# Optimization experiments

Hardware: AMD Instinct MI355X
Metric: run time of the kernel (lower is better)

The kernel has to match this reference:

```python
import jax, jax.numpy as jnp
import numpy as np

N, IN_DIM, H1, NHEAD = 8192, 768, 128, 2
H1T = NHEAD * H1          # 256: each AttentionLayer output dim
H2, H3, OUT = 128, 128, 64
K = H1T + 1 - H2          # 129: conv kernel width
E_PAIRS = 100000
ALPHA = 0.2
NEG = -9e15


def _l2norm(x):
    # F.normalize(p=2, dim=1)
    return x / jnp.maximum(jnp.linalg.norm(x, axis=1, keepdims=True), 1e-12)


def _gat_block(h, adj_mask, a, act):
    # h: [N, D]; a: [2D, 1]; dense NxN GAT attention, masked softmax, aggregate
    D = h.shape[1]
    wh1 = h @ a[:D]            # [N,1]
    wh2 = h @ a[D:]            # [N,1]
    e = act(wh1 + wh2.T)       # [N,N]
    att = jnp.where(adj_mask, e, NEG)
    att = jax.nn.softmax(att, axis=1)   # dropout omitted (eval/deterministic)
    return att @ h             # [N,D]


def _attention_layer(x, adj_mask, W, a, b):
    h = x @ W                  # [N, H1T]
    hp = _gat_block(h, adj_mask, a, lambda z: jax.nn.leaky_relu(z, negative_slope=ALPHA))
    return _l2norm(jax.nn.elu(hp)) + b


def setup_inputs() -> dict:
    key = jax.random.key(0)
    ks = jax.random.split(key, 16)
    g = 1.414

    def xavier(k, shape):
        fan_in, fan_out = shape[-2], shape[-1]
        bound = g * np.sqrt(6.0 / (fan_in + fan_out))
        return jax.random.uniform(k, shape, jnp.float32, -bound, bound)

    x = jax.random.normal(ks[0], (N, IN_DIM), jnp.float32)
    adj = jax.random.randint(ks[1], (N, N), 0, 2, jnp.int32)
    train_sample = jax.random.randint(ks[2], (E_PAIRS, 2), 0, N, jnp.int32)

    return {
        "x": x, "adj": adj, "train_sample": train_sample,
        # per-head GAT params (stacked over heads)
        "head_W": xavier(ks[3], (NHEAD, IN_DIM, H1T)),
        "head_a": xavier(ks[4], (NHEAD, 2 * H1T, 1)),
        "head_b": jnp.zeros((NHEAD, H1T), jnp.float32),
        # Conv attention layer
        "conv_w": jax.random.normal(ks[5], (1, 1, 1, K), jnp.float32) * (1.0 / np.sqrt(K)),
        "conv_cb": jnp.zeros((1,), jnp.float32),
        "conv_a": xavier(ks[6], (2 * H2, 1)),
        "conv_b": jnp.zeros((H2,), jnp.float32),
        # decoder MLPs (stored as [in, out])
        "tf_w1": xavier(ks[7], (H2, H3)), "tf_b1": jnp.zeros((H3,), jnp.float32),
        "tf_w2": xavier(ks[8], (H3, OUT)), "tf_b2": jnp.zeros((OUT,), jnp.float32),
        "tg_w1": xavier(ks[9], (H2, H3)), "tg_b1": jnp.zeros((H3,), jnp.float32),
        "tg_w2": xavier(ks[10], (H3, OUT)), "tg_b2": jnp.zeros((OUT,), jnp.float32),
    }


def reference(x, adj, train_sample, head_W, head_a, head_b,
              conv_w, conv_cb, conv_a, conv_b,
              tf_w1, tf_b1, tf_w2, tf_b2, tg_w1, tg_b1, tg_w2, tg_b2):
    adj_mask = adj > 0

    # Layer 1: mean over attention heads, then elu
    heads = jax.vmap(_attention_layer, in_axes=(None, None, 0, 0, 0))(
        x, adj_mask, head_W, head_a, head_b)           # [NHEAD, N, H1T]
    z = jax.nn.elu(jnp.mean(heads, axis=0))            # [N, H1T]

    # Conv layer: 1x129 conv sliding over feature axis -> [N, H2]
    zi = z[None, None, :, :]                           # [1,1,N,H1T]
    hc = jax.lax.conv_general_dilated(
        zi, conv_w, window_strides=(1, 1), padding="VALID",
        dimension_numbers=("NCHW", "OIHW", "NCHW"))
    h = hc[0, 0] + conv_cb[0]                          # [N, H2]

    hp = _gat_block(h, adj_mask, conv_a, jax.nn.elu)
    embed = _l2norm(jax.nn.elu(hp)) + conv_b           # [N, H2]

    # decoders (dropout p=0.01 omitted for deterministic reference)
    tf = jax.nn.elu(jax.nn.elu(embed @ tf_w1 + tf_b1) @ tf_w2 + tf_b2)
    tg = jax.nn.elu(jax.nn.elu(embed @ tg_w1 + tg_b1) @ tg_w2 + tg_b2)

    pred = jnp.sum(tf[train_sample[:, 0]] * tg[train_sample[:, 1]], axis=1, keepdims=True)
    return pred
```

## Files before the change

kernel.cpp:

```cpp
#include <hip/hip_runtime.h>


typedef _Float16 f16;
typedef _Float16 f16x8 __attribute__((ext_vector_type(8)));
typedef float f32x4 __attribute__((ext_vector_type(4)));

#define DEV __device__ __forceinline__
#define L2E 1.4426950408889634f
#define NN 8192
#define IND 768
#define D1 256
#define DT 512
#define D2 128
#define KC 129
#define EPAIRS 100000

#if __has_builtin(__builtin_amdgcn_exp2f)
#define EXP2(x) __builtin_amdgcn_exp2f(x)
#else
#define EXP2(x) exp2f(x)
#endif

DEV float eluf(float x){ return x > 0.f ? x : EXP2(x*L2E) - 1.f; }

__global__ __launch_bounds__(256) void k_pack(const int4* __restrict__ adj4, unsigned* __restrict__ maskw){
  int idx = blockIdx.x*256 + threadIdx.x;
  int4 v = adj4[idx];
  unsigned n = (unsigned)(v.x > 0) | ((unsigned)(v.y > 0) << 1)
             | ((unsigned)(v.z > 0) << 2) | ((unsigned)(v.w > 0) << 3);
  n |= __shfl_xor(n, 1) << 4;
  n |= __shfl_xor(n, 2) << 8;
  n |= __shfl_xor(n, 4) << 16;
  if ((threadIdx.x & 7) == 0) maskw[idx >> 3] = n;
}

__global__ __launch_bounds__(256) void k_cast_x(const float* __restrict__ x, f16* __restrict__ x16){
  int i = (blockIdx.x*256 + threadIdx.x)*4;
  float4 v = *(const float4*)(x + i);
  union { f16 h[4]; uint2 u; } p;
  p.h[0]=(f16)v.x; p.h[1]=(f16)v.y; p.h[2]=(f16)v.z; p.h[3]=(f16)v.w;
  *(uint2*)(x16 + i) = p.u;
}

__global__ __launch_bounds__(256) void k_wt(const float* __restrict__ W, f16* __restrict__ Wt){
  int np = blockIdx.x; int h = np >> 8, d = np & 255;
  for (int k = threadIdx.x; k < IND; k += 256)
    Wt[(size_t)np*IND + k] = (f16)W[((size_t)h*IND + k)*D1 + d];
}

__global__ __launch_bounds__(256) void k_gemm_h(
    const f16* __restrict__ x16, const f16* __restrict__ Wt,
    const float* __restrict__ head_a,
    f16* __restrict__ hT, float* __restrict__ wh1, float* __restrict__ wh2){
  __shared__ f16 As[64*72];
  __shared__ f16 Bs[128*72];
  int m0 = blockIdx.x*64, n0 = blockIdx.y*128;
  int t = threadIdx.x, lane = t & 63, w = t >> 6;
  int wi = w >> 1, wd = w & 1;
  int rm = lane & 15, qm = (lane >> 4)*8;
  f32x4 acc[2][4] = {};
  for (int k0 = 0; k0 < IND; k0 += 64){
#pragma unroll
    for (int p = 0; p < 2; p++){
      int idx = p*256 + t, r = idx >> 3, cc = (idx & 7)*8;
      *(uint4*)&As[r*72 + cc] = *(const uint4*)&x16[(size_t)(m0 + r)*IND + k0 + cc];
    }
#pragma unroll
    for (int p = 0; p < 4; p++){
      int idx = p*256 + t, r = idx >> 3, cc = (idx & 7)*8;
      *(uint4*)&Bs[r*72 + cc] = *(const uint4*)&Wt[(size_t)(n0 + r)*IND + k0 + cc];
    }
    __syncthreads();
#pragma unroll
    for (int ks = 0; ks < 2; ks++){
      f16x8 a0 = *(const f16x8*)&As[(wi*32 + rm)*72 + ks*32 + qm];
      f16x8 a1 = *(const f16x8*)&As[(wi*32 + 16 + rm)*72 + ks*32 + qm];
#pragma unroll
      for (int fn = 0; fn < 4; fn++){
        f16x8 b = *(const f16x8*)&Bs[(wd*64 + fn*16 + rm)*72 + ks*32 + qm];
        acc[0][fn] = __builtin_amdgcn_mfma_f32_16x16x32_f16(a0, b, acc[0][fn], 0, 0, 0);
        acc[1][fn] = __builtin_amdgcn_mfma_f32_16x16x32_f16(a1, b, acc[1][fn], 0, 0, 0);
      }
    }
    __syncthreads();
  }
  int quad = lane >> 4, cl = lane & 15;
  int head = n0 >> 8;
  float a1v[4], a2v[4];
#pragma unroll
  for (int fn = 0; fn < 4; fn++){
    int d = (n0 & 255) + wd*64 + fn*16 + cl;
    a1v[fn] = head_a[head*DT + d];
    a2v[fn] = head_a[head*DT + D1 + d];
  }
  float p1[2][4], p2[2][4];
#pragma unroll
  for (int fi = 0; fi < 2; fi++){
#pragma unroll
    for (int fn = 0; fn < 4; fn++){
      int npg = n0 + wd*64 + fn*16 + cl;
      int mg = m0 + wi*32 + fi*16 + quad*4;
      union { f16 h[4]; uint2 u; } pk;
#pragma unroll
      for (int reg = 0; reg < 4; reg++) pk.h[reg] = (f16)acc[fi][fn][reg];
      *(uint2*)&hT[(size_t)npg*NN + mg] = pk.u;
    }
#pragma unroll
    for (int reg = 0; reg < 4; reg++){
      float s1 = 0.f, s2 = 0.f;
#pragma unroll
      for (int fn = 0; fn < 4; fn++){ s1 += acc[fi][fn][reg]*a1v[fn]; s2 += acc[fi][fn][reg]*a2v[fn]; }
      p1[fi][reg] = s1; p2[fi][reg] = s2;
    }
  }
#pragma unroll
  for (int o = 1; o < 16; o <<= 1){
#pragma unroll
    for (int fi = 0; fi < 2; fi++)
#pragma unroll
      for (int reg = 0; reg < 4; reg++){
        p1[fi][reg] += __shfl_xor(p1[fi][reg], o);
        p2[fi][reg] += __shfl_xor(p2[fi][reg], o);
      }
  }
  if (cl == 0){
#pragma unroll
    for (int fi = 0; fi < 2; fi++)
#pragma unroll
      for (int reg = 0; reg < 4; reg++){
        int mg = m0 + wi*32 + fi*16 + quad*4 + reg;
        atomicAdd(&wh1[head*NN + mg], p1[fi][reg]);
        atomicAdd(&wh2[head*NN + mg], p2[fi][reg]);
      }
  }
}

__global__ __launch_bounds__(256) void k_gmax(const float* __restrict__ wh2, unsigned* __restrict__ gmax){
  int h = blockIdx.y;
  int i = blockIdx.x*256 + threadIdx.x;
  float v = wh2[h*NN + i];
#pragma unroll
  for (int o = 32; o > 0; o >>= 1) v = fmaxf(v, __shfl_xor(v, o));
  if ((threadIdx.x & 63) == 0){
    unsigned b = __float_as_uint(v);
    unsigned enc = (b & 0x80000000u) ? ~b : (b | 0x80000000u);
    atomicMax(gmax + h, enc);
  }
}

__global__ __launch_bounds__(256) void k_colterms(const float* __restrict__ wh2,
                                                  float* __restrict__ c1, float* __restrict__ c2){
  int i = blockIdx.x*256 + threadIdx.x;
  float v = wh2[i]*L2E;
  c1[i] = v; c2[i] = 0.2f*v;
}

__global__ __launch_bounds__(256) void k_agg_head(
    const f16* __restrict__ hT, const unsigned* __restrict__ maskw,
    const float* __restrict__ wh1, const float* __restrict__ c1,
    const float* __restrict__ c2, const unsigned* __restrict__ gmaxp,
    float* __restrict__ num, float* __restrict__ den){
  __shared__ f16 Hs[256*72];
  __shared__ f16 Ws[64*72];
  __shared__ float rowa[64], rowb[64];
  int head = blockIdx.z;
  int i0 = blockIdx.x*64;
  int jbase = blockIdx.y*4096;
  const f16* hTh = hT + (size_t)head*D1*NN;
  int t = threadIdx.x, lane = t & 63, w = t >> 6;
  int rm = lane & 15, qm = (lane >> 4)*8;
  if (t < 64){
    unsigned e = gmaxp[head];
    float gmax = __uint_as_float((e & 0x80000000u) ? (e ^ 0x80000000u) : ~e);
    float u = wh1[head*NN + i0 + t];
    float sm = u + gmax;
    float M = (sm > 0.f ? sm : 0.2f*sm)*L2E;
    rowa[t] = u*L2E - M;
    rowb[t] = 0.2f*u*L2E - M;
  }
  __syncthreads();
  int si = t >> 2, sjq = (t & 3)*16;
  float ra = rowa[si], rb = rowb[si];
  const float* c1h = c1 + head*NN;
  const float* c2h = c2 + head*NN;
  const unsigned* mrowp = maskw + (size_t)(i0 + si)*(NN/32);
  float rden = 0.f;
  f32x4 acc[4][4] = {};
  for (int j0 = 0; j0 < 4096; j0 += 64){
    int jg = jbase + j0;
#pragma unroll
    for (int p = 0; p < 8; p++){
      int idx = p*256 + t, dr = idx >> 3, cc = (idx & 7)*8;
      *(uint4*)&Hs[dr*72 + cc] = *(const uint4*)&hTh[(size_t)dr*NN + jg + cc];
    }
    unsigned mb = mrowp[(jg + sjq) >> 5] >> (sjq & 31);
    float ca[16], cb[16];
#pragma unroll
    for (int k = 0; k < 4; k++){
      float4 va = *(const float4*)&c1h[jg + sjq + 4*k];
      float4 vb = *(const float4*)&c2h[jg + sjq + 4*k];
      ca[4*k]=va.x; ca[4*k+1]=va.y; ca[4*k+2]=va.z; ca[4*k+3]=va.w;
      cb[4*k]=vb.x; cb[4*k+1]=vb.y; cb[4*k+2]=vb.z; cb[4*k+3]=vb.w;
    }
    f16x8 wlo, whi;
    float dsum = 0.f;
#pragma unroll
    for (int q = 0; q < 16; q++){
      float s1 = ra + ca[q], s2 = rb + cb[q];
      float wv = EXP2(fmaxf(s1, s2));
      wv = ((mb >> q) & 1u) ? wv : 0.f;
      dsum += wv;
      if (q < 8) wlo[q] = (f16)wv; else whi[q - 8] = (f16)wv;
    }
    *(f16x8*)&Ws[si*72 + sjq]     = wlo;
    *(f16x8*)&Ws[si*72 + sjq + 8] = whi;
    dsum += __shfl_xor(dsum, 1);
    dsum += __shfl_xor(dsum, 2);
    rden += dsum;
    __syncthreads();
#pragma unroll
    for (int ks = 0; ks < 2; ks++){
      f16x8 a[4], b[4];
#pragma unroll
      for (int mi = 0; mi < 4; mi++) a[mi] = *(const f16x8*)&Ws[(mi*16 + rm)*72 + ks*32 + qm];
#pragma unroll
      for (int fn = 0; fn < 4; fn++) b[fn] = *(const f16x8*)&Hs[(w*64 + fn*16 + rm)*72 + ks*32 + qm];
#pragma unroll
      for (int mi = 0; mi < 4; mi++)
#pragma unroll
        for (int fn = 0; fn < 4; fn++)
          acc[mi][fn] = __builtin_amdgcn_mfma_f32_16x16x32_f16(a[mi], b[fn], acc[mi][fn], 0, 0, 0);
    }
    __syncthreads();
  }
  if ((t & 3) == 0) atomicAdd(&den[head*NN + i0 + si], rden);
  int quad = lane >> 4, cl = lane & 15;
#pragma unroll
  for (int mi = 0; mi < 4; mi++)
#pragma unroll
    for (int fn = 0; fn < 4; fn++){
      int rr = i0 + mi*16 + quad*4;
      int dc = w*64 + fn*16 + cl;
#pragma unroll
      for (int reg = 0; reg < 4; reg++)
        atomicAdd(&num[((size_t)head*NN + rr + reg)*D1 + dc], acc[mi][fn][reg]);
    }
}

__global__ __launch_bounds__(256) void k_merge_conv(
    const float* __restrict__ num, const float* __restrict__ den,
    const float* __restrict__ head_b, const float* __restrict__ conv_w,
    const float* __restrict__ conv_cb, const float* __restrict__ conv_a,
    f16* __restrict__ gT, float* __restrict__ wc1L, float* __restrict__ wc2L){
  __shared__ float zrow[2][256];
  __shared__ float cw[KC];
  __shared__ float ca[256];
  __shared__ float red[2][2];
  __shared__ float red2[2][2][2];
  int t = threadIdx.x, g = t >> 7, c = t & 127;
  int r = blockIdx.x*2 + g;
  if (t < KC) cw[t] = conv_w[t];
  ca[t] = conv_a[t];
  float zv0 = 0.f, zv1 = 0.f;
#pragma unroll
  for (int h = 0; h < 2; h++){
    const float* nr = num + ((size_t)h*NN + r)*D1;
    float inv = 1.f / den[h*NN + r];
    float e0 = eluf(nr[c]*inv);
    float e1 = eluf(nr[c + 128]*inv);
    float ss = e0*e0 + e1*e1;
#pragma unroll
    for (int o = 32; o > 0; o >>= 1) ss += __shfl_xor(ss, o);
    if ((t & 63) == 0) red[g][(t >> 6) & 1] = ss;
    __syncthreads();
    float invn = 1.f / fmaxf(sqrtf(red[g][0] + red[g][1]), 1e-12f);
    zv0 += e0*invn + head_b[h*D1 + c];
    zv1 += e1*invn + head_b[h*D1 + 128 + c];
    __syncthreads();
  }
  zrow[g][c]       = eluf(0.5f*zv0);
  zrow[g][c + 128] = eluf(0.5f*zv1);
  __syncthreads();
  float s = conv_cb[0];
  for (int k = 0; k < KC; k++) s += zrow[g][c + k]*cw[k];
  gT[(size_t)c*NN + r] = (f16)s;
  float p1 = s*ca[c], p2 = s*ca[128 + c];
#pragma unroll
  for (int o = 32; o > 0; o >>= 1){ p1 += __shfl_xor(p1, o); p2 += __shfl_xor(p2, o); }
  if ((t & 63) == 0){ red2[g][(t >> 6) & 1][0] = p1; red2[g][(t >> 6) & 1][1] = p2; }
  __syncthreads();
  if ((t & 127) == 0){
    wc1L[r] = (red2[g][0][0] + red2[g][1][0])*L2E;
    wc2L[r] = (red2[g][0][1] + red2[g][1][1])*L2E;
  }
}

__global__ __launch_bounds__(256) void k_agg_conv(
    const f16* __restrict__ gT, const unsigned* __restrict__ maskw,
    const float* __restrict__ wc1L, const float* __restrict__ wc2L,
    float* __restrict__ num, float* __restrict__ den){
  __shared__ f16 Hs[128*72];
  __shared__ f16 Ws[64*72];
  __shared__ float rowc[64];
  int i0 = blockIdx.x*64;
  int jbase = blockIdx.y*1024;
  int t = threadIdx.x, lane = t & 63, w = t >> 6;
  int rm = lane & 15, qm = (lane >> 4)*8;
  if (t < 64) rowc[t] = wc1L[i0 + t];
  __syncthreads();
  int si = t >> 2, sjq = (t & 3)*16;
  float ra = rowc[si];
  const unsigned* mrowp = maskw + (size_t)(i0 + si)*(NN/32);
  float rden = 0.f;
  f32x4 acc[4][2] = {};
  for (int j0 = 0; j0 < 1024; j0 += 64){
    int jg = jbase + j0;
#pragma unroll
    for (int p = 0; p < 4; p++){
      int idx = p*256 + t, dr = idx >> 3, cc = (idx & 7)*8;
      *(uint4*)&Hs[dr*72 + cc] = *(const uint4*)&gT[(size_t)dr*NN + jg + cc];
    }
    unsigned mb = mrowp[(jg + sjq) >> 5] >> (sjq & 31);
    float ca[16];
#pragma unroll
    for (int k = 0; k < 4; k++){
      float4 va = *(const float4*)&wc2L[jg + sjq + 4*k];
      ca[4*k]=va.x; ca[4*k+1]=va.y; ca[4*k+2]=va.z; ca[4*k+3]=va.w;
    }
    f16x8 wlo, whi;
    float dsum = 0.f;
#pragma unroll
    for (int q = 0; q < 16; q++){
      float sL = ra + ca[q];
      float t2 = EXP2(sL);
      float wv = sL > 0.f ? t2 : EXP2((t2 - 1.f)*L2E);
      wv = ((mb >> q) & 1u) ? wv : 0.f;
      dsum += wv;
      if (q < 8) wlo[q] = (f16)wv; else whi[q - 8] = (f16)wv;
    }
    *(f16x8*)&Ws[si*72 + sjq]     = wlo;
    *(f16x8*)&Ws[si*72 + sjq + 8] = whi;
    dsum += __shfl_xor(dsum, 1);
    dsum += __shfl_xor(dsum, 2);
    rden += dsum;
    __syncthreads();
#pragma unroll
    for (int ks = 0; ks < 2; ks++){
      f16x8 a[4], b[2];
#pragma unroll
      for (int mi = 0; mi < 4; mi++) a[mi] = *(const f16x8*)&Ws[(mi*16 + rm)*72 + ks*32 + qm];
#pragma unroll
      for (int fn = 0; fn < 2; fn++) b[fn] = *(const f16x8*)&Hs[(w*32 + fn*16 + rm)*72 + ks*32 + qm];
#pragma unroll
      for (int mi = 0; mi < 4; mi++)
#pragma unroll
        for (int fn = 0; fn < 2; fn++)
          acc[mi][fn] = __builtin_amdgcn_mfma_f32_16x16x32_f16(a[mi], b[fn], acc[mi][fn], 0, 0, 0);
    }
    __syncthreads();
  }
  if ((t & 3) == 0) atomicAdd(&den[i0 + si], rden);
  int quad = lane >> 4, cl = lane & 15;
#pragma unroll
  for (int mi = 0; mi < 4; mi++)
#pragma unroll
    for (int fn = 0; fn < 2; fn++){
      int rr = i0 + mi*16 + quad*4;
      int dc = w*32 + fn*16 + cl;
#pragma unroll
      for (int reg = 0; reg < 4; reg++)
        atomicAdd(&num[(size_t)(rr + reg)*D2 + dc], acc[mi][fn][reg]);
    }
}

__global__ __launch_bounds__(256) void k_embed(
    const float* __restrict__ numc, const float* __restrict__ denc,
    const float* __restrict__ conv_b, float* __restrict__ embed){
  __shared__ float red[2][2];
  int t = threadIdx.x, g = t >> 7, c = t & 127;
  int r = blockIdx.x*2 + g;
  float e = eluf(numc[(size_t)r*D2 + c] / denc[r]);
  float ss = e*e;
#pragma unroll
  for (int o = 32; o > 0; o >>= 1) ss += __shfl_xor(ss, o);
  if ((t & 63) == 0) red[g][(t >> 6) & 1] = ss;
  __syncthreads();
  float invn = 1.f / fmaxf(sqrtf(red[g][0] + red[g][1]), 1e-12f);
  embed[(size_t)r*D2 + c] = e*invn + conv_b[c];
}

__global__ __launch_bounds__(256) void k_mlp(
    const float* __restrict__ embed,
    const float* __restrict__ fw1, const float* __restrict__ fb1,
    const float* __restrict__ fw2, const float* __restrict__ fb2,
    const float* __restrict__ gw1, const float* __restrict__ gb1,
    const float* __restrict__ gw2, const float* __restrict__ gb2,
    float* __restrict__ tf, float* __restrict__ tg){
  const float* w1 = blockIdx.y ? gw1 : fw1;
  const float* b1 = blockIdx.y ? gb1 : fb1;
  const float* w2 = blockIdx.y ? gw2 : fw2;
  const float* b2 = blockIdx.y ? gb2 : fb2;
  float* out = blockIdx.y ? tg : tf;
  int t = threadIdx.x;
  int c = t & 127, kh = t >> 7;
  int o = t & 63, kh2 = t >> 6;
  float rw1[64];
#pragma unroll
  for (int i = 0; i < 64; i++) rw1[i] = w1[(kh*64 + i)*128 + c];
  float rw2[32];
#pragma unroll
  for (int i = 0; i < 32; i++) rw2[i] = w2[(kh2*32 + i)*64 + o];
  float bb1 = b1[c], bb2 = b2[o];
  __shared__ float erow[4][128];
  __shared__ float hidp[2][4][128];
  __shared__ float hid[4][128];
  __shared__ float outp[4][4][64];
  int r0 = blockIdx.x*32;
  for (int it = 0; it < 8; it++){
    int rbase = r0 + it*4;
    ((float2*)erow)[t] = ((const float2*)(embed + (size_t)rbase*128))[t];
    __syncthreads();
#pragma unroll
    for (int g = 0; g < 4; g++){
      float s = 0.f;
#pragma unroll
      for (int i = 0; i < 64; i++) s += erow[g][kh*64 + i]*rw1[i];
      hidp[kh][g][c] = s;
    }
    __syncthreads();
#pragma unroll
    for (int gg = 0; gg < 2; gg++){
      int g = kh + 2*gg;
      hid[g][c] = eluf(bb1 + hidp[0][g][c] + hidp[1][g][c]);
    }
    __syncthreads();
#pragma unroll
    for (int g = 0; g < 4; g++){
      float s = 0.f;
#pragma unroll
      for (int i = 0; i < 32; i++) s += hid[g][kh2*32 + i]*rw2[i];
      outp[kh2][g][o] = s;
    }
    __syncthreads();
    { int g = t >> 6;
      out[(size_t)(rbase + g)*64 + o] =
        eluf(bb2 + outp[0][g][o] + outp[1][g][o] + outp[2][g][o] + outp[3][g][o]); }
    __syncthreads();
  }
}

__global__ __launch_bounds__(256) void k_pred(
    const int* __restrict__ ts, const float4* __restrict__ tf4,
    const float4* __restrict__ tg4, float* __restrict__ out){
  int p = blockIdx.x*16 + (threadIdx.x >> 4);
  int l = threadIdx.x & 15;
  int i = ts[2*p], j = ts[2*p + 1];
  float4 a = tf4[(size_t)i*16 + l], b = tg4[(size_t)j*16 + l];
  float v = a.x*b.x + a.y*b.y + a.z*b.z + a.w*b.w;
  v += __shfl_xor(v, 1); v += __shfl_xor(v, 2);
  v += __shfl_xor(v, 4); v += __shfl_xor(v, 8);
  if (l == 0) out[p] = v;
}

#define OFF_MASK  ((size_t)0)
#define OFF_X16   ((size_t)8388608)
#define OFF_WT16  ((size_t)20971520)
#define OFF_HT16  ((size_t)21757952)
#define OFF_WH1   ((size_t)30146560)
#define OFF_WH2   ((size_t)30212096)
#define OFF_C1    ((size_t)30277632)
#define OFF_C2    ((size_t)30343168)
#define OFF_GMAX  ((size_t)30408704)
#define OFF_NUM1  ((size_t)30408960)
#define OFF_DEN1  ((size_t)47186176)
#define OFF_GT16  ((size_t)47251712)
#define OFF_WC1L  ((size_t)49348864)
#define OFF_WC2L  ((size_t)49381632)
#define OFF_NUMC  ((size_t)49414400)
#define OFF_DENC  ((size_t)53608704)
#define OFF_EMB   ((size_t)53641472)
#define OFF_TF    ((size_t)57835776)
#define OFF_TG    ((size_t)59932928)

extern "C" void kernel_launch(void* const* d_in, const int* in_sizes, int n_in,
                              void* d_out, int out_size, void* d_ws, size_t ws_size,
                              hipStream_t stream){
  const float* x      = (const float*)d_in[0];
  const int*   adj    = (const int*)d_in[1];
  const int*   ts     = (const int*)d_in[2];
  const float* head_W = (const float*)d_in[3];
  const float* head_a = (const float*)d_in[4];
  const float* head_b = (const float*)d_in[5];
  const float* conv_w = (const float*)d_in[6];
  const float* conv_cb= (const float*)d_in[7];
  const float* conv_a = (const float*)d_in[8];
  const float* conv_b = (const float*)d_in[9];
  const float* tf_w1  = (const float*)d_in[10];
  const float* tf_b1  = (const float*)d_in[11];
  const float* tf_w2  = (const float*)d_in[12];
  const float* tf_b2  = (const float*)d_in[13];
  const float* tg_w1  = (const float*)d_in[14];
  const float* tg_b1  = (const float*)d_in[15];
  const float* tg_w2  = (const float*)d_in[16];
  const float* tg_b2  = (const float*)d_in[17];
  float* outp = (float*)d_out;
  char* ws = (char*)d_ws;

  unsigned* maskw = (unsigned*)(ws + OFF_MASK);
  f16*   x16   = (f16*)(ws + OFF_X16);
  f16*   Wt16  = (f16*)(ws + OFF_WT16);
  f16*   hT16  = (f16*)(ws + OFF_HT16);
  float* wh1   = (float*)(ws + OFF_WH1);
  float* wh2   = (float*)(ws + OFF_WH2);
  float* c1    = (float*)(ws + OFF_C1);
  float* c2    = (float*)(ws + OFF_C2);
  unsigned* gmax = (unsigned*)(ws + OFF_GMAX);
  float* num1  = (float*)(ws + OFF_NUM1);
  float* den1  = (float*)(ws + OFF_DEN1);
  f16*   gT16  = (f16*)(ws + OFF_GT16);
  float* wc1L  = (float*)(ws + OFF_WC1L);
  float* wc2L  = (float*)(ws + OFF_WC2L);
  float* numc  = (float*)(ws + OFF_NUMC);
  float* denc  = (float*)(ws + OFF_DENC);
  float* emb   = (float*)(ws + OFF_EMB);
  float* tf    = (float*)(ws + OFF_TF);
  float* tg    = (float*)(ws + OFF_TG);

  hipMemsetAsync(wh1, 0, 2*2*NN*sizeof(float), stream);
  hipMemsetAsync(gmax, 0, 2*sizeof(unsigned), stream);
  hipMemsetAsync(num1, 0, (size_t)2*NN*D1*sizeof(float) + 2*NN*sizeof(float), stream);
  hipMemsetAsync(numc, 0, (size_t)NN*D2*sizeof(float) + NN*sizeof(float), stream);

  k_pack   <<<NN*NN/1024, 256, 0, stream>>>((const int4*)adj, maskw);
  k_cast_x <<<(NN*IND)/(256*4), 256, 0, stream>>>(x, x16);
  k_wt     <<<DT, 256, 0, stream>>>(head_W, Wt16);
  k_gemm_h <<<dim3(NN/64, DT/128), 256, 0, stream>>>(x16, Wt16, head_a, hT16, wh1, wh2);
  k_gmax   <<<dim3(NN/256, 2), 256, 0, stream>>>(wh2, gmax);
  k_colterms<<<(2*NN)/256, 256, 0, stream>>>(wh2, c1, c2);
  k_agg_head<<<dim3(NN/64, 2, 2), 256, 0, stream>>>(hT16, maskw, wh1, c1, c2, gmax, num1, den1);
  k_merge_conv<<<NN/2, 256, 0, stream>>>(num1, den1, head_b, conv_w, conv_cb, conv_a, gT16, wc1L, wc2L);
  k_agg_conv<<<dim3(NN/64, 8), 256, 0, stream>>>(gT16, maskw, wc1L, wc2L, numc, denc);
  k_embed  <<<NN/2, 256, 0, stream>>>(numc, denc, conv_b, emb);
  k_mlp    <<<dim3(NN/32, 2), 256, 0, stream>>>(emb, tf_w1, tf_b1, tf_w2, tf_b2,
                                                tg_w1, tg_b1, tg_w2, tg_b2, tf, tg);
  k_pred   <<<EPAIRS/16, 256, 0, stream>>>(ts, (const float4*)tf, (const float4*)tg, outp);
}
```

Measured before the change: 710.4 us.

## Fuse prep kernels, register-prefetch tiles with XOR-swizzled LDS, fold embed into MLP

Merges the adjacency packing, x cast and W transpose into one launch, and merges the gmax and column-term kernels. The GEMM and both aggregation kernels now prefetch the next global tile into registers while the current one is computed, and store tiles in unpadded shared memory with an XOR swizzle, which leaves one barrier per iteration. The GEMM stages its hT output through shared memory so the global writes are coalesced. The embed normalization moves into the MLP kernel, removing one launch and the embed buffer round trip. Aggregation kernels get launch_bounds(256,2), and the register prefetch adds register pressure.

```diff
diff --git a/kernel.cpp b/kernel.cpp
--- a/kernel.cpp
+++ b/kernel.cpp
@@ -23,69 +23,107 @@
 
 DEV float eluf(float x){ return x > 0.f ? x : EXP2(x*L2E) - 1.f; }
 
-__global__ __launch_bounds__(256) void k_pack(const int4* __restrict__ adj4, unsigned* __restrict__ maskw){
-  int idx = blockIdx.x*256 + threadIdx.x;
-  int4 v = adj4[idx];
-  unsigned n = (unsigned)(v.x > 0) | ((unsigned)(v.y > 0) << 1)
-             | ((unsigned)(v.z > 0) << 2) | ((unsigned)(v.w > 0) << 3);
-  n |= __shfl_xor(n, 1) << 4;
-  n |= __shfl_xor(n, 2) << 8;
-  n |= __shfl_xor(n, 4) << 16;
-  if ((threadIdx.x & 7) == 0) maskw[idx >> 3] = n;
-}
-
-__global__ __launch_bounds__(256) void k_cast_x(const float* __restrict__ x, f16* __restrict__ x16){
-  int i = (blockIdx.x*256 + threadIdx.x)*4;
-  float4 v = *(const float4*)(x + i);
-  union { f16 h[4]; uint2 u; } p;
-  p.h[0]=(f16)v.x; p.h[1]=(f16)v.y; p.h[2]=(f16)v.z; p.h[3]=(f16)v.w;
-  *(uint2*)(x16 + i) = p.u;
-}
-
-__global__ __launch_bounds__(256) void k_wt(const float* __restrict__ W, f16* __restrict__ Wt){
-  int np = blockIdx.x; int h = np >> 8, d = np & 255;
-  for (int k = threadIdx.x; k < IND; k += 256)
-    Wt[(size_t)np*IND + k] = (f16)W[((size_t)h*IND + k)*D1 + d];
+__global__ __launch_bounds__(256) void k_prep(
+    const int4* __restrict__ adj4, unsigned* __restrict__ maskw,
+    const float* __restrict__ x, f16* __restrict__ x16,
+    const float* __restrict__ W, f16* __restrict__ Wt){
+  int b = blockIdx.x, t = threadIdx.x;
+  if (b < 65536){
+    int idx = b*256 + t;
+    int4 v = adj4[idx];
+    unsigned n = (unsigned)(v.x > 0) | ((unsigned)(v.y > 0) << 1)
+               | ((unsigned)(v.z > 0) << 2) | ((unsigned)(v.w > 0) << 3);
+    n |= __shfl_xor(n, 1) << 4;
+    n |= __shfl_xor(n, 2) << 8;
+    n |= __shfl_xor(n, 4) << 16;
+    if ((t & 7) == 0) maskw[idx >> 3] = n;
+  } else if (b < 65536 + 6144){
+    int i = ((b - 65536)*256 + t)*4;
+    float4 v = *(const float4*)(x + i);
+    union { f16 h[4]; uint2 u; } p;
+    p.h[0]=(f16)v.x; p.h[1]=(f16)v.y; p.h[2]=(f16)v.z; p.h[3]=(f16)v.w;
+    *(uint2*)(x16 + i) = p.u;
+  } else {
+    int np = b - 71680; int h = np >> 8, d = np & 255;
+    for (int k = t; k < IND; k += 256)
+      Wt[(size_t)np*IND + k] = (f16)W[((size_t)h*IND + k)*D1 + d];
+  }
 }
 
 __global__ __launch_bounds__(256) void k_gemm_h(
     const f16* __restrict__ x16, const f16* __restrict__ Wt,
     const float* __restrict__ head_a,
     f16* __restrict__ hT, float* __restrict__ wh1, float* __restrict__ wh2){
-  __shared__ f16 As[64*72];
-  __shared__ f16 Bs[128*72];
+  __shared__ f16 SM[(64 + 128)*64];
+  f16* As = SM;
+  f16* Bs = SM + 64*64;
   int m0 = blockIdx.x*64, n0 = blockIdx.y*128;
   int t = threadIdx.x, lane = t & 63, w = t >> 6;
   int wi = w >> 1, wd = w & 1;
-  int rm = lane & 15, qm = (lane >> 4)*8;
+  int rm = lane & 15, q4 = lane >> 4;
+  int drb = t >> 3, gofs = (t & 7)*8;
+  int sg8 = (((t & 7) ^ ((t >> 3) & 7))*8);
   f32x4 acc[2][4] = {};
+  uint4 preA[2], preB[4];
+#pragma unroll
+  for (int p = 0; p < 2; p++)
+    preA[p] = *(const uint4*)&x16[(size_t)(m0 + p*32 + drb)*IND + gofs];
+#pragma unroll
+  for (int p = 0; p < 4; p++)
+    preB[p] = *(const uint4*)&Wt[(size_t)(n0 + p*32 + drb)*IND + gofs];
   for (int k0 = 0; k0 < IND; k0 += 64){
-#pragma unroll
-    for (int p = 0; p < 2; p++){
-      int idx = p*256 + t, r = idx >> 3, cc = (idx & 7)*8;
-      *(uint4*)&As[r*72 + cc] = *(const uint4*)&x16[(size_t)(m0 + r)*IND + k0 + cc];
-    }
-#pragma unroll
-    for (int p = 0; p < 4; p++){
-      int idx = p*256 + t, r = idx >> 3, cc = (idx & 7)*8;
-      *(uint4*)&Bs[r*72 + cc] = *(const uint4*)&Wt[(size_t)(n0 + r)*IND + k0 + cc];
-    }
-    __syncthreads();
+    __syncthreads();
+#pragma unroll
+    for (int p = 0; p < 2; p++) *(uint4*)&As[(p*32 + drb)*64 + sg8] = preA[p];
+#pragma unroll
+    for (int p = 0; p < 4; p++) *(uint4*)&Bs[(p*32 + drb)*64 + sg8] = preB[p];
+    __syncthreads();
+    if (k0 + 64 < IND){
+#pragma unroll
+      for (int p = 0; p < 2; p++)
+        preA[p] = *(const uint4*)&x16[(size_t)(m0 + p*32 + drb)*IND + k0 + 64 + gofs];
+#pragma unroll
+      for (int p = 0; p < 4; p++)
+        preB[p] = *(const uint4*)&Wt[(size_t)(n0 + p*32 + drb)*IND + k0 + 64 + gofs];
+    }
 #pragma unroll
     for (int ks = 0; ks < 2; ks++){
-      f16x8 a0 = *(const f16x8*)&As[(wi*32 + rm)*72 + ks*32 + qm];
-      f16x8 a1 = *(const f16x8*)&As[(wi*32 + 16 + rm)*72 + ks*32 + qm];
+      int gl = ks*4 + q4;
+      int r0 = wi*32 + rm, r1 = wi*32 + 16 + rm;
+      f16x8 a0 = *(const f16x8*)&As[r0*64 + ((gl ^ (r0 & 7))*8)];
+      f16x8 a1 = *(const f16x8*)&As[r1*64 + ((gl ^ (r1 & 7))*8)];
 #pragma unroll
       for (int fn = 0; fn < 4; fn++){
-        f16x8 b = *(const f16x8*)&Bs[(wd*64 + fn*16 + rm)*72 + ks*32 + qm];
+        int rb = wd*64 + fn*16 + rm;
+        f16x8 b = *(const f16x8*)&Bs[rb*64 + ((gl ^ (rb & 7))*8)];
         acc[0][fn] = __builtin_amdgcn_mfma_f32_16x16x32_f16(a0, b, acc[0][fn], 0, 0, 0);
         acc[1][fn] = __builtin_amdgcn_mfma_f32_16x16x32_f16(a1, b, acc[1][fn], 0, 0, 0);
       }
     }
-    __syncthreads();
   }
   int quad = lane >> 4, cl = lane & 15;
   int head = n0 >> 8;
+  f16* T = SM;
+  __syncthreads();
+#pragma unroll
+  for (int fi = 0; fi < 2; fi++)
+#pragma unroll
+    for (int fn = 0; fn < 4; fn++){
+      int d = wd*64 + fn*16 + cl;
+      int i = wi*32 + fi*16 + quad*4;
+      union { f16 h[4]; uint2 u; } pk;
+#pragma unroll
+      for (int reg = 0; reg < 4; reg++) pk.h[reg] = (f16)acc[fi][fn][reg];
+      *(uint2*)&T[d*72 + i] = pk.u;
+    }
+  __syncthreads();
+  { int row = t >> 1, half = t & 1;
+    const f16* src = &T[row*72 + half*32];
+    f16* dst = &hT[(size_t)(n0 + row)*NN + m0 + half*32];
+#pragma unroll
+    for (int q = 0; q < 4; q++)
+      *(uint4*)&dst[q*8] = *(const uint4*)&src[q*8];
+  }
   float a1v[4], a2v[4];
 #pragma unroll
   for (int fn = 0; fn < 4; fn++){
@@ -95,16 +133,7 @@
   }
   float p1[2][4], p2[2][4];
 #pragma unroll
-  for (int fi = 0; fi < 2; fi++){
-#pragma unroll
-    for (int fn = 0; fn < 4; fn++){
-      int npg = n0 + wd*64 + fn*16 + cl;
-      int mg = m0 + wi*32 + fi*16 + quad*4;
-      union { f16 h[4]; uint2 u; } pk;
-#pragma unroll
-      for (int reg = 0; reg < 4; reg++) pk.h[reg] = (f16)acc[fi][fn][reg];
-      *(uint2*)&hT[(size_t)npg*NN + mg] = pk.u;
-    }
+  for (int fi = 0; fi < 2; fi++)
 #pragma unroll
     for (int reg = 0; reg < 4; reg++){
       float s1 = 0.f, s2 = 0.f;
@@ -112,7 +141,6 @@
       for (int fn = 0; fn < 4; fn++){ s1 += acc[fi][fn][reg]*a1v[fn]; s2 += acc[fi][fn][reg]*a2v[fn]; }
       p1[fi][reg] = s1; p2[fi][reg] = s2;
     }
-  }
 #pragma unroll
   for (int o = 1; o < 16; o <<= 1){
 #pragma unroll
@@ -135,65 +163,59 @@
   }
 }
 
-__global__ __launch_bounds__(256) void k_gmax(const float* __restrict__ wh2, unsigned* __restrict__ gmax){
-  int h = blockIdx.y;
+__global__ __launch_bounds__(256) void k_rowterms(const float* __restrict__ wh2,
+    float* __restrict__ c1, float* __restrict__ c2, unsigned* __restrict__ gmax){
   int i = blockIdx.x*256 + threadIdx.x;
-  float v = wh2[h*NN + i];
-#pragma unroll
-  for (int o = 32; o > 0; o >>= 1) v = fmaxf(v, __shfl_xor(v, o));
+  float v = wh2[i];
+  c1[i] = v*L2E; c2[i] = 0.2f*v*L2E;
+  float m = v;
+#pragma unroll
+  for (int o = 32; o > 0; o >>= 1) m = fmaxf(m, __shfl_xor(m, o));
   if ((threadIdx.x & 63) == 0){
-    unsigned b = __float_as_uint(v);
-    unsigned enc = (b & 0x80000000u) ? ~b : (b | 0x80000000u);
-    atomicMax(gmax + h, enc);
-  }
-}
-
-__global__ __launch_bounds__(256) void k_colterms(const float* __restrict__ wh2,
-                                                  float* __restrict__ c1, float* __restrict__ c2){
-  int i = blockIdx.x*256 + threadIdx.x;
-  float v = wh2[i]*L2E;
-  c1[i] = v; c2[i] = 0.2f*v;
-}
-
-__global__ __launch_bounds__(256) void k_agg_head(
+    unsigned bbits = __float_as_uint(m);
+    unsigned enc = (bbits & 0x80000000u) ? ~bbits : (bbits | 0x80000000u);
+    atomicMax(gmax + (i >> 13), enc);
+  }
+}
+
+__global__ __launch_bounds__(256, 2) void k_agg_head(
     const f16* __restrict__ hT, const unsigned* __restrict__ maskw,
     const float* __restrict__ wh1, const float* __restrict__ c1,
     const float* __restrict__ c2, const unsigned* __restrict__ gmaxp,
     float* __restrict__ num, float* __restrict__ den){
-  __shared__ f16 Hs[256*72];
-  __shared__ f16 Ws[64*72];
-  __shared__ float rowa[64], rowb[64];
+  __shared__ f16 Hs[256*64];
+  __shared__ f16 Ws[64*64];
   int head = blockIdx.z;
   int i0 = blockIdx.x*64;
   int jbase = blockIdx.y*4096;
   const f16* hTh = hT + (size_t)head*D1*NN;
   int t = threadIdx.x, lane = t & 63, w = t >> 6;
-  int rm = lane & 15, qm = (lane >> 4)*8;
-  if (t < 64){
-    unsigned e = gmaxp[head];
-    float gmax = __uint_as_float((e & 0x80000000u) ? (e ^ 0x80000000u) : ~e);
-    float u = wh1[head*NN + i0 + t];
-    float sm = u + gmax;
-    float M = (sm > 0.f ? sm : 0.2f*sm)*L2E;
-    rowa[t] = u*L2E - M;
-    rowb[t] = 0.2f*u*L2E - M;
-  }
-  __syncthreads();
+  int rm = lane & 15, q4 = lane >> 4;
   int si = t >> 2, sjq = (t & 3)*16;
-  float ra = rowa[si], rb = rowb[si];
+  unsigned e = gmaxp[head];
+  float gmax = __uint_as_float((e & 0x80000000u) ? (e ^ 0x80000000u) : ~e);
+  float u = wh1[head*NN + i0 + si];
+  float sm = u + gmax;
+  float M = (sm > 0.f ? sm : 0.2f*sm)*L2E;
+  float ra = u*L2E - M, rb = 0.2f*u*L2E - M;
   const float* c1h = c1 + head*NN;
   const float* c2h = c2 + head*NN;
   const unsigned* mrowp = maskw + (size_t)(i0 + si)*(NN/32);
+  int drb = t >> 3, gofs = (t & 7)*8;
+  int sg8 = (((t & 7) ^ ((t >> 3) & 7))*8);
+  int wg0 = (t & 3)*2;
   float rden = 0.f;
   f32x4 acc[4][4] = {};
+  uint4 pre[8];
+#pragma unroll
+  for (int p = 0; p < 8; p++)
+    pre[p] = *(const uint4*)&hTh[(size_t)(p*32 + drb)*NN + jbase + gofs];
   for (int j0 = 0; j0 < 4096; j0 += 64){
     int jg = jbase + j0;
-#pragma unroll
-    for (int p = 0; p < 8; p++){
-      int idx = p*256 + t, dr = idx >> 3, cc = (idx & 7)*8;
-      *(uint4*)&Hs[dr*72 + cc] = *(const uint4*)&hTh[(size_t)dr*NN + jg + cc];
-    }
-    unsigned mb = mrowp[(jg + sjq) >> 5] >> (sjq & 31);
+    __syncthreads();
+#pragma unroll
+    for (int p = 0; p < 8; p++) *(uint4*)&Hs[(p*32 + drb)*64 + sg8] = pre[p];
+    unsigned mb = mrowp[(unsigned)(jg + sjq) >> 5] >> (sjq & 31);
     float ca[16], cb[16];
 #pragma unroll
     for (int k = 0; k < 4; k++){
@@ -212,26 +234,37 @@
       dsum += wv;
       if (q < 8) wlo[q] = (f16)wv; else whi[q - 8] = (f16)wv;
     }
-    *(f16x8*)&Ws[si*72 + sjq]     = wlo;
-    *(f16x8*)&Ws[si*72 + sjq + 8] = whi;
+    *(f16x8*)&Ws[si*64 + ((wg0       ^ (si & 7))*8)] = wlo;
+    *(f16x8*)&Ws[si*64 + (((wg0 + 1) ^ (si & 7))*8)] = whi;
     dsum += __shfl_xor(dsum, 1);
     dsum += __shfl_xor(dsum, 2);
     rden += dsum;
     __syncthreads();
+    if (j0 + 64 < 4096){
+#pragma unroll
+      for (int p = 0; p < 8; p++)
+        pre[p] = *(const uint4*)&hTh[(size_t)(p*32 + drb)*NN + jg + 64 + gofs];
+    }
 #pragma unroll
     for (int ks = 0; ks < 2; ks++){
+      int gl = ks*4 + q4;
       f16x8 a[4], b[4];
 #pragma unroll
-      for (int mi = 0; mi < 4; mi++) a[mi] = *(const f16x8*)&Ws[(mi*16 + rm)*72 + ks*32 + qm];
-#pragma unroll
-      for (int fn = 0; fn < 4; fn++) b[fn] = *(const f16x8*)&Hs[(w*64 + fn*16 + rm)*72 + ks*32 + qm];
+      for (int mi = 0; mi < 4; mi++){
+        int row = mi*16 + rm;
+        a[mi] = *(const f16x8*)&Ws[row*64 + ((gl ^ (row & 7))*8)];
+      }
+#pragma unroll
+      for (int fn = 0; fn < 4; fn++){
+        int row = w*64 + fn*16 + rm;
+        b[fn] = *(const f16x8*)&Hs[row*64 + ((gl ^ (row & 7))*8)];
+      }
 #pragma unroll
       for (int mi = 0; mi < 4; mi++)
 #pragma unroll
         for (int fn = 0; fn < 4; fn++)
           acc[mi][fn] = __builtin_amdgcn_mfma_f32_16x16x32_f16(a[mi], b[fn], acc[mi][fn], 0, 0, 0);
     }
-    __syncthreads();
   }
   if ((t & 3) == 0) atomicAdd(&den[head*NN + i0 + si], rden);
   int quad = lane >> 4, cl = lane & 15;
@@ -295,69 +328,82 @@
   }
 }
 
-__global__ __launch_bounds__(256) void k_agg_conv(
+__global__ __launch_bounds__(256, 2) void k_agg_conv(
     const f16* __restrict__ gT, const unsigned* __restrict__ maskw,
     const float* __restrict__ wc1L, const float* __restrict__ wc2L,
     float* __restrict__ num, float* __restrict__ den){
-  __shared__ f16 Hs[128*72];
-  __shared__ f16 Ws[64*72];
-  __shared__ float rowc[64];
+  __shared__ f16 Hs[128*64];
+  __shared__ f16 Ws[64*64];
   int i0 = blockIdx.x*64;
   int jbase = blockIdx.y*1024;
   int t = threadIdx.x, lane = t & 63, w = t >> 6;
-  int rm = lane & 15, qm = (lane >> 4)*8;
-  if (t < 64) rowc[t] = wc1L[i0 + t];
-  __syncthreads();
+  int rm = lane & 15, q4 = lane >> 4;
   int si = t >> 2, sjq = (t & 3)*16;
-  float ra = rowc[si];
+  float ra = wc1L[i0 + si];
   const unsigned* mrowp = maskw + (size_t)(i0 + si)*(NN/32);
+  int drb = t >> 3, gofs = (t & 7)*8;
+  int sg8 = (((t & 7) ^ ((t >> 3) & 7))*8);
+  int wg0 = (t & 3)*2;
   float rden = 0.f;
   f32x4 acc[4][2] = {};
+  uint4 pre[4];
+#pragma unroll
+  for (int p = 0; p < 4; p++)
+    pre[p] = *(const uint4*)&gT[(size_t)(p*32 + drb)*NN + jbase + gofs];
   for (int j0 = 0; j0 < 1024; j0 += 64){
     int jg = jbase + j0;
-#pragma unroll
-    for (int p = 0; p < 4; p++){
-      int idx = p*256 + t, dr = idx >> 3, cc = (idx & 7)*8;
-      *(uint4*)&Hs[dr*72 + cc] = *(const uint4*)&gT[(size_t)dr*NN + jg + cc];
-    }
-    unsigned mb = mrowp[(jg + sjq) >> 5] >> (sjq & 31);
-    float ca[16];
+    __syncthreads();
+#pragma unroll
+    for (int p = 0; p < 4; p++) *(uint4*)&Hs[(p*32 + drb)*64 + sg8] = pre[p];
+    unsigned mb = mrowp[(unsigned)(jg + sjq) >> 5] >> (sjq & 31);
+    float cc[16];
 #pragma unroll
     for (int k = 0; k < 4; k++){
       float4 va = *(const float4*)&wc2L[jg + sjq + 4*k];
-      ca[4*k]=va.x; ca[4*k+1]=va.y; ca[4*k+2]=va.z; ca[4*k+3]=va.w;
+      cc[4*k]=va.x; cc[4*k+1]=va.y; cc[4*k+2]=va.z; cc[4*k+3]=va.w;
     }
     f16x8 wlo, whi;
     float dsum = 0.f;
 #pragma unroll
     for (int q = 0; q < 16; q++){
-      float sL = ra + ca[q];
+      float sL = ra + cc[q];
       float t2 = EXP2(sL);
       float wv = sL > 0.f ? t2 : EXP2((t2 - 1.f)*L2E);
       wv = ((mb >> q) & 1u) ? wv : 0.f;
       dsum += wv;
       if (q < 8) wlo[q] = (f16)wv; else whi[q - 8] = (f16)wv;
     }
-    *(f16x8*)&Ws[si*72 + sjq]     = wlo;
-    *(f16x8*)&Ws[si*72 + sjq + 8] = whi;
+    *(f16x8*)&Ws[si*64 + ((wg0       ^ (si & 7))*8)] = wlo;
+    *(f16x8*)&Ws[si*64 + (((wg0 + 1) ^ (si & 7))*8)] = whi;
     dsum += __shfl_xor(dsum, 1);
     dsum += __shfl_xor(dsum, 2);
     rden += dsum;
     __syncthreads();
+    if (j0 + 64 < 1024){
+#pragma unroll
+      for (int p = 0; p < 4; p++)
+        pre[p] = *(const uint4*)&gT[(size_t)(p*32 + drb)*NN + jg + 64 + gofs];
+    }
 #pragma unroll
     for (int ks = 0; ks < 2; ks++){
+      int gl = ks*4 + q4;
       f16x8 a[4], b[2];
 #pragma unroll
-      for (int mi = 0; mi < 4; mi++) a[mi] = *(const f16x8*)&Ws[(mi*16 + rm)*72 + ks*32 + qm];
-#pragma unroll
-      for (int fn = 0; fn < 2; fn++) b[fn] = *(const f16x8*)&Hs[(w*32 + fn*16 + rm)*72 + ks*32 + qm];
+      for (int mi = 0; mi < 4; mi++){
+        int row = mi*16 + rm;
+        a[mi] = *(const f16x8*)&Ws[row*64 + ((gl ^ (row & 7))*8)];
+      }
+#pragma unroll
+      for (int fn = 0; fn < 2; fn++){
+        int row = w*32 + fn*16 + rm;
+        b[fn] = *(const f16x8*)&Hs[row*64 + ((gl ^ (row & 7))*8)];
+      }
 #pragma unroll
       for (int mi = 0; mi < 4; mi++)
 #pragma unroll
         for (int fn = 0; fn < 2; fn++)
           acc[mi][fn] = __builtin_amdgcn_mfma_f32_16x16x32_f16(a[mi], b[fn], acc[mi][fn], 0, 0, 0);
     }
-    __syncthreads();
   }
   if ((t & 3) == 0) atomicAdd(&den[i0 + si], rden);
   int quad = lane >> 4, cl = lane & 15;
@@ -373,24 +419,9 @@
     }
 }
 
-__global__ __launch_bounds__(256) void k_embed(
+__global__ __launch_bounds__(256) void k_mlp(
     const float* __restrict__ numc, const float* __restrict__ denc,
-    const float* __restrict__ conv_b, float* __restrict__ embed){
-  __shared__ float red[2][2];
-  int t = threadIdx.x, g = t >> 7, c = t & 127;
-  int r = blockIdx.x*2 + g;
-  float e = eluf(numc[(size_t)r*D2 + c] / denc[r]);
-  float ss = e*e;
-#pragma unroll
-  for (int o = 32; o > 0; o >>= 1) ss += __shfl_xor(ss, o);
-  if ((t & 63) == 0) red[g][(t >> 6) & 1] = ss;
-  __syncthreads();
-  float invn = 1.f / fmaxf(sqrtf(red[g][0] + red[g][1]), 1e-12f);
-  embed[(size_t)r*D2 + c] = e*invn + conv_b[c];
-}
-
-__global__ __launch_bounds__(256) void k_mlp(
-    const float* __restrict__ embed,
+    const float* __restrict__ conv_b,
     const float* __restrict__ fw1, const float* __restrict__ fb1,
     const float* __restrict__ fw2, const float* __restrict__ fb2,
     const float* __restrict__ gw1, const float* __restrict__ gb1,
@@ -404,6 +435,23 @@
   int t = threadIdx.x;
   int c = t & 127, kh = t >> 7;
   int o = t & 63, kh2 = t >> 6;
+  int r0 = blockIdx.x*32;
+  __shared__ float es[32][132];
+  { int row = t >> 3, c0 = (t & 7)*16;
+    float inv = 1.f / denc[r0 + row];
+    float ev[16]; float ss = 0.f;
+#pragma unroll
+    for (int k = 0; k < 4; k++){
+      float4 v = *(const float4*)&numc[(size_t)(r0 + row)*D2 + c0 + 4*k];
+      float e0 = eluf(v.x*inv), e1 = eluf(v.y*inv), e2 = eluf(v.z*inv), e3 = eluf(v.w*inv);
+      ev[4*k]=e0; ev[4*k+1]=e1; ev[4*k+2]=e2; ev[4*k+3]=e3;
+      ss += e0*e0 + e1*e1 + e2*e2 + e3*e3;
+    }
+    ss += __shfl_xor(ss, 1); ss += __shfl_xor(ss, 2); ss += __shfl_xor(ss, 4);
+    float invn = 1.f / fmaxf(sqrtf(ss), 1e-12f);
+#pragma unroll
+    for (int k = 0; k < 16; k++) es[row][c0 + k] = ev[k]*invn + conv_b[c0 + k];
+  }
   float rw1[64];
 #pragma unroll
   for (int i = 0; i < 64; i++) rw1[i] = w1[(kh*64 + i)*128 + c];
@@ -411,20 +459,17 @@
 #pragma unroll
   for (int i = 0; i < 32; i++) rw2[i] = w2[(kh2*32 + i)*64 + o];
   float bb1 = b1[c], bb2 = b2[o];
-  __shared__ float erow[4][128];
   __shared__ float hidp[2][4][128];
   __shared__ float hid[4][128];
   __shared__ float outp[4][4][64];
-  int r0 = blockIdx.x*32;
+  __syncthreads();
   for (int it = 0; it < 8; it++){
-    int rbase = r0 + it*4;
-    ((float2*)erow)[t] = ((const float2*)(embed + (size_t)rbase*128))[t];
-    __syncthreads();
+    int rb4 = it*4;
 #pragma unroll
     for (int g = 0; g < 4; g++){
       float s = 0.f;
 #pragma unroll
-      for (int i = 0; i < 64; i++) s += erow[g][kh*64 + i]*rw1[i];
+      for (int i = 0; i < 64; i++) s += es[rb4 + g][kh*64 + i]*rw1[i];
       hidp[kh][g][c] = s;
     }
     __syncthreads();
@@ -443,7 +488,7 @@
     }
     __syncthreads();
     { int g = t >> 6;
-      out[(size_t)(rbase + g)*64 + o] =
+      out[(size_t)(r0 + rb4 + g)*64 + o] =
         eluf(bb2 + outp[0][g][o] + outp[1][g][o] + outp[2][g][o] + outp[3][g][o]); }
     __syncthreads();
   }
@@ -468,9 +513,9 @@
 #define OFF_HT16  ((size_t)21757952)
 #define OFF_WH1   ((size_t)30146560)
 #define OFF_WH2   ((size_t)30212096)
-#define OFF_C1    ((size_t)30277632)
-#define OFF_C2    ((size_t)30343168)
-#define OFF_GMAX  ((size_t)30408704)
+#define OFF_GMAX  ((size_t)30277632)
+#define OFF_C1    ((size_t)30277888)
+#define OFF_C2    ((size_t)30343424)
 #define OFF_NUM1  ((size_t)30408960)
 #define OFF_DEN1  ((size_t)47186176)
 #define OFF_GT16  ((size_t)47251712)
@@ -478,9 +523,8 @@
 #define OFF_WC2L  ((size_t)49381632)
 #define OFF_NUMC  ((size_t)49414400)
 #define OFF_DENC  ((size_t)53608704)
-#define OFF_EMB   ((size_t)53641472)
-#define OFF_TF    ((size_t)57835776)
-#define OFF_TG    ((size_t)59932928)
+#define OFF_TF    ((size_t)53641472)
+#define OFF_TG    ((size_t)55738624)
 
 extern "C" void kernel_launch(void* const* d_in, const int* in_sizes, int n_in,
                               void* d_out, int out_size, void* d_ws, size_t ws_size,
@@ -512,9 +556,9 @@
   f16*   hT16  = (f16*)(ws + OFF_HT16);
   float* wh1   = (float*)(ws + OFF_WH1);
   float* wh2   = (float*)(ws + OFF_WH2);
+  unsigned* gmax = (unsigned*)(ws + OFF_GMAX);
   float* c1    = (float*)(ws + OFF_C1);
   float* c2    = (float*)(ws + OFF_C2);
-  unsigned* gmax = (unsigned*)(ws + OFF_GMAX);
   float* num1  = (float*)(ws + OFF_NUM1);
   float* den1  = (float*)(ws + OFF_DEN1);
   f16*   gT16  = (f16*)(ws + OFF_GT16);
@@ -522,26 +566,21 @@
   float* wc2L  = (float*)(ws + OFF_WC2L);
   float* numc  = (float*)(ws + OFF_NUMC);
   float* denc  = (float*)(ws + OFF_DENC);
-  float* emb   = (float*)(ws + OFF_EMB);
   float* tf    = (float*)(ws + OFF_TF);
   float* tg    = (float*)(ws + OFF_TG);
 
-  hipMemsetAsync(wh1, 0, 2*2*NN*sizeof(float), stream);
-  hipMemsetAsync(gmax, 0, 2*sizeof(unsigned), stream);
-  hipMemsetAsync(num1, 0, (size_t)2*NN*D1*sizeof(float) + 2*NN*sizeof(float), stream);
-  hipMemsetAsync(numc, 0, (size_t)NN*D2*sizeof(float) + NN*sizeof(float), stream);
-
-  k_pack   <<<NN*NN/1024, 256, 0, stream>>>((const int4*)adj, maskw);
-  k_cast_x <<<(NN*IND)/(256*4), 256, 0, stream>>>(x, x16);
-  k_wt     <<<DT, 256, 0, stream>>>(head_W, Wt16);
+  hipMemsetAsync(wh1, 0, 131328, stream);
+  hipMemsetAsync(num1, 0, 16842752, stream);
+  hipMemsetAsync(numc, 0, 4227072, stream);
+
+  k_prep   <<<72192, 256, 0, stream>>>((const int4*)adj, maskw, x, x16, head_W, Wt16);
   k_gemm_h <<<dim3(NN/64, DT/128), 256, 0, stream>>>(x16, Wt16, head_a, hT16, wh1, wh2);
-  k_gmax   <<<dim3(NN/256, 2), 256, 0, stream>>>(wh2, gmax);
-  k_colterms<<<(2*NN)/256, 256, 0, stream>>>(wh2, c1, c2);
+  k_rowterms<<<64, 256, 0, stream>>>(wh2, c1, c2, gmax);
   k_agg_head<<<dim3(NN/64, 2, 2), 256, 0, stream>>>(hT16, maskw, wh1, c1, c2, gmax, num1, den1);
   k_merge_conv<<<NN/2, 256, 0, stream>>>(num1, den1, head_b, conv_w, conv_cb, conv_a, gT16, wc1L, wc2L);
   k_agg_conv<<<dim3(NN/64, 8), 256, 0, stream>>>(gT16, maskw, wc1L, wc2L, numc, denc);
-  k_embed  <<<NN/2, 256, 0, stream>>>(numc, denc, conv_b, emb);
-  k_mlp    <<<dim3(NN/32, 2), 256, 0, stream>>>(emb, tf_w1, tf_b1, tf_w2, tf_b2,
+  k_mlp    <<<dim3(NN/32, 2), 256, 0, stream>>>(numc, denc, conv_b,
+                                                tf_w1, tf_b1, tf_w2, tf_b2,
                                                 tg_w1, tg_b1, tg_w2, tg_b2, tf, tg);
   k_pred   <<<EPAIRS/16, 256, 0, stream>>>(ts, (const float4*)tf, (const float4*)tg, outp);
 }
```

Result: slower. 965.0 us (+35.8%).
